# Performance work log

Measured on AMD Instinct MI355X. Metric: run time of the kernel, lower is better.

Reference implementation:

```python
import jax, jax.numpy as jnp
import numpy as np
from jax import lax

_DN = ('NCHW', 'OIHW', 'NCHW')


def _depthwise_kernel(C):
    base = jnp.array([[0.1, 0.1, 0.1], [0.1, 0.2, 0.1], [0.1, 0.1, 0.1]], jnp.float32)
    return jnp.broadcast_to(base[None, None], (C, 1, 3, 3))


def setup_inputs() -> dict:
    key = jax.random.key(0)
    k0, k1, k2 = jax.random.split(key, 3)
    T, B, C, H, W = 16, 16, 8, 128, 128
    hidden = max(1, C // 16)  # reduction_ratio = 16
    events = jax.random.normal(k0, (T, B, C, H, W), jnp.float32)
    conv_w = _depthwise_kernel(C)  # fixed neighbor kernel from _initialize_weights
    att_w1 = jax.random.normal(k1, (hidden, 2 * C), jnp.float32) / np.sqrt(2 * C)
    att_w2 = jax.random.normal(k2, (C, hidden), jnp.float32) / np.sqrt(hidden)
    return {
        'events': events,
        'conv_w': conv_w,
        'att_w1': att_w1,
        'att_w2': att_w2,
        'density_w': jnp.array(1.0, jnp.float32),
        'temporal_w': jnp.array(0.8, jnp.float32),
        'motion_w': jnp.array(0.5, jnp.float32),
    }


def _forward(events, conv_w, att_w1, att_w2, density_w, temporal_w, motion_w):
    T, B, C, H, W = events.shape
    x = events.reshape(T * B, C, H, W)
    # depthwise 3x3 neighbor conv (groups=C), batched over all T steps at once
    wi = lax.conv_general_dilated(x, conv_w, (1, 1), 'SAME',
                                  dimension_numbers=_DN, feature_group_count=C)
    # --- BALIFBetaAdaptor: max/avg pool -> 1x1 convs (== matmuls) -> sigmoid ---
    mx = jnp.max(x, axis=(2, 3))            # (TB, C)
    av = jnp.mean(x, axis=(2, 3))           # (TB, C)
    pooled = jnp.concatenate([mx, av], axis=1)  # (TB, 2C)
    h = jax.nn.relu(pooled @ att_w1.T)
    beta = (0.5 + 0.45 * jax.nn.sigmoid(h @ att_w2.T)).reshape(T, B, C, 1, 1)
    # --- LightweightEventAdaptor: density / temporal change / unfold variance ---
    density = jnp.mean(x, axis=(1, 2, 3)).reshape(T, B)
    diff = jnp.mean(jnp.abs(events[1:] - events[:-1]), axis=(2, 3, 4))
    temporal = jnp.concatenate([jnp.zeros((1, B), events.dtype), diff], axis=0)  # t=0 -> 0
    # F.unfold(k=3,pad=1) variance over dim=1 (C*9 values, unbiased) via sum-convs
    ones_k = jnp.ones((1, C, 3, 3), events.dtype)
    s1 = lax.conv_general_dilated(x, ones_k, (1, 1), 'SAME', dimension_numbers=_DN)
    s2 = lax.conv_general_dilated(x * x, ones_k, (1, 1), 'SAME', dimension_numbers=_DN)
    n = C * 9
    var = (s2 - s1 * s1 / n) / (n - 1)      # (TB,1,H,W), matches torch.var (ddof=1)
    motion = jnp.mean(var, axis=(1, 2, 3)).reshape(T, B)
    adj = jax.nn.sigmoid(density_w * density + temporal_w * temporal + motion_w * motion) * 2.0
    thr = (1.0 + adj).reshape(T, B, 1, 1, 1)  # base_threshold = 1.0
    wi = wi.reshape(T, B, C, H, W)

    # --- sequential LIF charge/fire/reset (torch.no_grad -> stop_gradient) ---
    def step(v, inp):
        w, b, th, cur = inp
        v = lax.stop_gradient(b * v + (1.0 - b) * w)              # charge
        spike = lax.stop_gradient(jnp.arctan(2.0 * (v - th)) * 0.5 + 0.5)  # atan surrogate
        v = lax.stop_gradient((1.0 - spike) * v)                  # reset (v_reset = 0)
        return v, cur * spike

    v0 = jnp.zeros((B, C, H, W), events.dtype)
    _, out = lax.scan(step, v0, (wi, beta, thr, events))
    return out  # (T,B,C,H,W)


def reference(events, conv_w, att_w1, att_w2, density_w, temporal_w, motion_w):
    return _forward(events, conv_w, att_w1, att_w2, density_w, temporal_w, motion_w)
```

## Files before the change

kernel.cpp:

```cpp
#include <hip/hip_runtime.h>
#include <math.h>

#define T_ 16
#define B_ 16
#define C_ 8
#define H_ 128
#define W_ 128
#define HW_ (H_*W_)
#define CHW_ (C_*HW_)
#define TC 4
#define NSL 16

__device__ __forceinline__ float wave_sum(float v){
    #pragma unroll
    for (int o=32;o>0;o>>=1) v += __shfl_down(v,o,64);
    return v;
}
__device__ __forceinline__ float wave_max(float v){
    #pragma unroll
    for (int o=32;o>0;o>>=1) v = fmaxf(v,__shfl_down(v,o,64));
    return v;
}

__global__ __launch_bounds__(512, 4) void stats_kernel(
    const float* __restrict__ events, float* __restrict__ partials,
    float* __restrict__ yfield)
{
    int bid   = blockIdx.x;
    int chunk = bid & 3;
    int s     = (bid >> 2) & 15;
    int b     = bid >> 6;
    int t0    = chunk * TC;
    int gh0   = s * 8;
    int tid   = threadIdx.x;
    int c     = tid >> 6;
    int lane  = tid & 63;

    __shared__ float xs[C_][1024];

    int lrow  = lane >> 3;
    int lcol0 = (lane & 7) * 16;
    int gh    = gh0 + lrow;
    float cnth = (gh==0 || gh==H_-1) ? 2.f : 3.f;
    float w0  = (lcol0==0)        ? 2.f : 3.f;
    float w15 = (lcol0+15==W_-1)  ? 2.f : 3.f;

    const float* base0 = events + (size_t)(t0*B_+b)*CHW_ + c*HW_ + gh*W_ + lcol0;
    const size_t tstep = (size_t)B_ * CHW_;

    float px[16];
    if (t0 > 0){
        const float* pp = base0 - tstep;
        #pragma unroll
        for (int e=0;e<16;e+=4){
            float4 v = *reinterpret_cast<const float4*>(pp + e);
            px[e]=v.x; px[e+1]=v.y; px[e+2]=v.z; px[e+3]=v.w;
        }
    } else {
        #pragma unroll
        for (int e=0;e<16;e++) px[e]=0.f;
    }

    #pragma unroll 1
    for (int tt=0; tt<TC; ++tt){
        int t = t0 + tt;
        const float* src = base0 + (size_t)tt*tstep;

        float cx[16];
        #pragma unroll
        for (int e=0;e<16;e+=4){
            float4 v = *reinterpret_cast<const float4*>(src + e);
            cx[e]=v.x; cx[e+1]=v.y; cx[e+2]=v.z; cx[e+3]=v.w;
        }

        float ssum=0.f, smax=-INFINITY, q=0.f, dsu=0.f;
        #pragma unroll
        for (int e=0;e<16;e++){
            float x = cx[e];
            ssum += x;
            smax = fmaxf(smax, x);
            float w = (e==0) ? w0 : ((e==15) ? w15 : 3.f);
            q = fmaf(w*x, x, q);
            dsu += fabsf(x - px[e]);
            px[e] = x;
        }

        #pragma unroll
        for (int e=0;e<16;e+=4){
            float4 v; v.x=cx[e]; v.y=cx[e+1]; v.z=cx[e+2]; v.w=cx[e+3];
            *reinterpret_cast<float4*>(&xs[c][lane*16 + e]) = v;
        }
        __syncthreads();

        {
            int p0 = tid * 2;
            float y0=0.f, y1=0.f;
            #pragma unroll
            for (int cc=0; cc<C_; cc++){
                y0 += xs[cc][p0];
                y1 += xs[cc][p0+1];
            }
            float2 yy; yy.x=y0; yy.y=y1;
            *reinterpret_cast<float2*>(yfield + (size_t)(t*B_+b)*HW_ + gh0*W_ + p0) = yy;
        }

        float rs = wave_sum(ssum);
        float rm = wave_max(smax);
        float rd = wave_sum(dsu);
        float rq = wave_sum(cnth * q);
        if (lane == 0){
            float4 o; o.x=rs; o.y=rm; o.z=rd; o.w=rq;
            *reinterpret_cast<float4*>(
                partials + (((size_t)(t*B_+b)*NSL + s)*C_ + c)*4) = o;
        }
        __syncthreads();
    }
}

__global__ __launch_bounds__(256) void m1_kernel(
    const float* __restrict__ yfield, float* __restrict__ m1p)
{
    int bid = blockIdx.x;
    int s   = bid & 7;
    int tb  = bid >> 3;
    int h0  = s*16;
    int tid = threadIdx.x;
    __shared__ float yb[18][W_];

    const float* yf = yfield + (size_t)tb*HW_;
    for (int i = tid; i < 18*32; i += 256){
        int rr = i >> 5, cc = (i & 31) * 4;
        int gh = h0 - 1 + rr;
        float4 v; v.x=0.f; v.y=0.f; v.z=0.f; v.w=0.f;
        if (gh >= 0 && gh < H_) v = *reinterpret_cast<const float4*>(yf + gh*W_ + cc);
        *reinterpret_cast<float4*>(&yb[rr][cc]) = v;
    }
    __syncthreads();

    float m1 = 0.f;
    {
        int w  = tid & 127;
        int rg = tid >> 7;
        bool hasL = (w>0), hasR = (w<W_-1);
        int base = rg*8;
        const float* row;
        row = yb[base];   float a0 = row[w] + (hasL?row[w-1]:0.f) + (hasR?row[w+1]:0.f);
        row = yb[base+1]; float a1 = row[w] + (hasL?row[w-1]:0.f) + (hasR?row[w+1]:0.f);
        #pragma unroll
        for (int i=0;i<8;i++){
            row = yb[base+2+i];
            float a2 = row[w] + (hasL?row[w-1]:0.f) + (hasR?row[w+1]:0.f);
            float s1 = a0 + a1 + a2;
            m1 = fmaf(s1, s1, m1);
            a0 = a1; a1 = a2;
        }
    }
    m1 = wave_sum(m1);
    __shared__ float red2[4];
    int lane = tid & 63, wv = tid >> 6;
    if (lane==0) red2[wv] = m1;
    __syncthreads();
    if (tid==0) m1p[bid] = (red2[0]+red2[1])+(red2[2]+red2[3]);
}

__global__ __launch_bounds__(64) void combine_kernel(
    const float* __restrict__ partials,
    const float* __restrict__ m1p,
    const float* __restrict__ att_w1,
    const float* __restrict__ att_w2,
    const float* __restrict__ dwp, const float* __restrict__ twp,
    const float* __restrict__ mwp,
    float* __restrict__ beta_out, float* __restrict__ thr_out,
    float* __restrict__ zeropad)
{
    int tb = blockIdx.x;
    int t  = tb / B_;
    int i  = threadIdx.x;
    if (tb == 0 && i < 16) zeropad[i] = 0.f;
    __shared__ float v[19];
    const float* p = partials + (size_t)tb*NSL*C_*4;
    if (i < 8){
        float acc = 0.f;
        #pragma unroll
        for (int s=0;s<NSL;s++) acc += p[(s*C_ + i)*4 + 0];
        v[i] = acc;
    } else if (i < 16){
        int c = i - 8;
        float acc = -INFINITY;
        #pragma unroll
        for (int s=0;s<NSL;s++) acc = fmaxf(acc, p[(s*C_ + c)*4 + 1]);
        v[i] = acc;
    } else if (i == 16){
        float acc = 0.f;
        for (int k=0;k<NSL*C_;k++) acc += p[k*4 + 2];
        v[16] = acc;
    } else if (i == 17){
        const float* mp = m1p + (size_t)tb*8;
        float acc = 0.f;
        #pragma unroll
        for (int k=0;k<8;k++) acc += mp[k];
        v[17] = acc;
    } else if (i == 18){
        float acc = 0.f;
        for (int k=0;k<NSL*C_;k++) acc += p[k*4 + 3];
        v[18] = acc;
    }
    __syncthreads();
    if (i == 0){
        float h1 = 0.f;
        for (int c=0;c<C_;c++) h1 += v[8+c] * att_w1[c];
        for (int c=0;c<C_;c++) h1 += (v[c]/(float)HW_) * att_w1[C_+c];
        h1 = fmaxf(h1, 0.f);
        float total = 0.f;
        for (int c=0;c<C_;c++) total += v[c];
        float density  = total / (float)CHW_;
        float temporal = (t==0) ? 0.f : v[16] / (float)CHW_;
        float motion   = (v[18] - v[17]/72.f) / 71.f / (float)HW_;
        float z = dwp[0]*density + twp[0]*temporal + mwp[0]*motion;
        float adj = 2.f / (1.f + expf(-z));
        thr_out[tb] = 1.f + adj;
        for (int c=0;c<C_;c++){
            float sg = 1.f / (1.f + expf(-(h1 * att_w2[c])));
            beta_out[tb*C_ + c] = 0.5f + 0.45f*sg;
        }
    }
}

__device__ __forceinline__ void gload16(const float* src, float* lds_dst){
    __builtin_amdgcn_global_load_lds(
        (const __attribute__((address_space(1))) unsigned int*)src,
        (__attribute__((address_space(3))) unsigned int*)lds_dst, 16, 0, 0);
}

__device__ __forceinline__ float fast_atan(float x){
    float ax = fabsf(x);
    bool inv = ax > 1.f;
    float z  = inv ? __builtin_amdgcn_rcpf(ax) : ax;
    float z2 = z*z;
    float p = -0.0117212f;
    p = fmaf(p, z2,  0.05265332f);
    p = fmaf(p, z2, -0.11643287f);
    p = fmaf(p, z2,  0.19354346f);
    p = fmaf(p, z2, -0.33262347f);
    p = fmaf(p, z2,  0.99997726f);
    p = p * z;
    float r = inv ? (1.57079632679f - p) : p;
    return copysignf(r, x);
}

#define SROWS 10

__global__ __launch_bounds__(256, 8) void lif_kernel(
    const float* __restrict__ events,
    const float* __restrict__ conv_w,
    const float* __restrict__ beta,
    const float* __restrict__ thr,
    const float* __restrict__ zeropad,
    float* __restrict__ out)
{
    int bid  = blockIdx.x;
    int hblk = bid & 15;
    int bc   = bid >> 4;
    int b = bc >> 3, c = bc & 7;
    int h0 = hblk * 8;
    int tid = threadIdx.x;
    int wv  = tid >> 6;

    float wk[9];
    #pragma unroll
    for (int k=0;k<9;k++) wk[k] = conv_w[c*9 + k];

    __shared__ float lds[2][SROWS*W_];

    int idxA = tid,        rowA = idxA >> 5, colA = (idxA & 31) * 4;
    int idxB = 256 + tid,  rowB = idxB >> 5, colB = (idxB & 31) * 4;
    int ghA = h0 - 1 + rowA;
    int ghB = h0 - 1 + rowB;
    bool okA = (ghA >= 0) && (ghA < H_);
    bool okB = (ghB >= 0) && (ghB < H_);
    const float* baseFrame = events + ((size_t)(b * C_) + c) * HW_;
    const float* srcA0 = okA ? (baseFrame + ghA*W_ + colA) : zeropad;
    const float* srcB0 = okB ? (baseFrame + ghB*W_ + colB) : zeropad;
    const size_t tstep = (size_t)B_ * CHW_;
    size_t stepA = okA ? tstep : 0;
    size_t stepB = okB ? tstep : 0;

    int w  = tid & 127;
    int rg = tid >> 7;
    int rbase = rg * 4;
    int wl = (w > 0)    ? w-1 : 0;
    int wr = (w < W_-1) ? w+1 : W_-1;
    bool hasL = (w > 0), hasR = (w < W_-1);

    float v[4];
    #pragma unroll
    for (int i=0;i<4;i++) v[i] = 0.f;

    gload16(srcA0, &lds[0][wv*256]);
    if (wv == 0) gload16(srcB0, &lds[0][1024]);

    const float* bp = beta + (b*C_ + c);
    const float* tp = thr + b;
    float bv = bp[0];
    float th = tp[0];

    for (int t = 0; t < T_; ++t){
        int cur = t & 1, nxt = cur ^ 1;
        __syncthreads();

        if (t + 1 < T_){
            gload16(srcA0 + (size_t)(t+1)*stepA, &lds[nxt][wv*256]);
            if (wv == 0) gload16(srcB0 + (size_t)(t+1)*stepB, &lds[nxt][1024]);
        }
        float bvn = (t+1 < T_) ? bp[(size_t)(t+1)*B_*C_] : 0.f;
        float thn = (t+1 < T_) ? tp[(size_t)(t+1)*B_]    : 0.f;

        const float* L = &lds[cur][0];
        float omb = 1.f - bv;
        float* op = out + ((size_t)(t*B_+b)*C_ + c)*HW_ + h0*W_;

        const float* row0 = L + rbase*W_;
        const float* row1 = row0 + W_;
        float la = hasL ? row0[wl] : 0.f;  float ma = row0[w];  float ra = hasR ? row0[wr] : 0.f;
        float lb = hasL ? row1[wl] : 0.f;  float mb = row1[w];  float rb = hasR ? row1[wr] : 0.f;

        #pragma unroll
        for (int i=0;i<4;i++){
            const float* rowc = L + (rbase+2+i)*W_;
            float lc = hasL ? rowc[wl] : 0.f;
            float mc = rowc[w];
            float rc = hasR ? rowc[wr] : 0.f;
            float wi = wk[0]*la + wk[1]*ma + wk[2]*ra
                     + wk[3]*lb + wk[4]*mb + wk[5]*rb
                     + wk[6]*lc + wk[7]*mc + wk[8]*rc;
            float vv = fmaf(bv, v[i], omb*wi);
            float sp = fast_atan(2.f*(vv - th))*0.5f + 0.5f;
            __builtin_nontemporal_store(mb * sp, &op[(rbase+i)*W_ + w]);
            v[i] = (1.f - sp) * vv;
            la=lb; ma=mb; ra=rb; lb=lc; mb=mc; rb=rc;
        }
        __syncthreads();

        bv = bvn; th = thn;
    }
}

extern "C" void kernel_launch(void* const* d_in, const int* in_sizes, int n_in,
                              void* d_out, int out_size, void* d_ws, size_t ws_size,
                              hipStream_t stream)
{
    const float* events = (const float*)d_in[0];
    const float* conv_w = (const float*)d_in[1];
    const float* att_w1 = (const float*)d_in[2];
    const float* att_w2 = (const float*)d_in[3];
    const float* dwp    = (const float*)d_in[4];
    const float* twp    = (const float*)d_in[5];
    const float* mwp    = (const float*)d_in[6];
    float* out = (float*)d_out;

    float* ws       = (float*)d_ws;
    float* partials = ws;
    float* m1p      = partials + (size_t)T_*B_*NSL*C_*4;
    float* beta     = m1p + (size_t)T_*B_*8;
    float* thr      = beta + (size_t)T_*B_*C_;
    float* zeropad  = thr + T_*B_;
    float* yfield   = zeropad + 16;

    stats_kernel  <<<B_*NSL*4,  512, 0, stream>>>(events, partials, yfield);
    m1_kernel     <<<T_*B_*8,   256, 0, stream>>>(yfield, m1p);
    combine_kernel<<<T_*B_,     64,  0, stream>>>(partials, m1p, att_w1, att_w2,
                                                  dwp, twp, mwp, beta, thr, zeropad);
    lif_kernel    <<<B_*C_*16,  256, 0, stream>>>(events, conv_w, beta, thr, zeropad, out);
}
```

Measured before the change: 95.37 us.

## Restructure LIF kernel: register-prefetch triple-buffered LDS, float4 tiles, cheaper atan

```diff
diff --git a/kernel.cpp b/kernel.cpp
--- a/kernel.cpp
+++ b/kernel.cpp
@@ -10,6 +10,8 @@
 #define CHW_ (C_*HW_)
 #define TC 4
 #define NSL 16
+
+typedef float __attribute__((ext_vector_type(4))) f32x4;
 
 __device__ __forceinline__ float wave_sum(float v){
     #pragma unroll
@@ -170,13 +172,11 @@
     const float* __restrict__ att_w2,
     const float* __restrict__ dwp, const float* __restrict__ twp,
     const float* __restrict__ mwp,
-    float* __restrict__ beta_out, float* __restrict__ thr_out,
-    float* __restrict__ zeropad)
+    float* __restrict__ beta_out, float* __restrict__ thr_out)
 {
     int tb = blockIdx.x;
     int t  = tb / B_;
     int i  = threadIdx.x;
-    if (tb == 0 && i < 16) zeropad[i] = 0.f;
     __shared__ float v[19];
     const float* p = partials + (size_t)tb*NSL*C_*4;
     if (i < 8){
@@ -226,36 +226,27 @@
     }
 }
 
-__device__ __forceinline__ void gload16(const float* src, float* lds_dst){
-    __builtin_amdgcn_global_load_lds(
-        (const __attribute__((address_space(1))) unsigned int*)src,
-        (__attribute__((address_space(3))) unsigned int*)lds_dst, 16, 0, 0);
-}
-
-__device__ __forceinline__ float fast_atan(float x){
+__device__ __forceinline__ float fast_atan5(float x){
     float ax = fabsf(x);
     bool inv = ax > 1.f;
     float z  = inv ? __builtin_amdgcn_rcpf(ax) : ax;
     float z2 = z*z;
-    float p = -0.0117212f;
-    p = fmaf(p, z2,  0.05265332f);
-    p = fmaf(p, z2, -0.11643287f);
-    p = fmaf(p, z2,  0.19354346f);
-    p = fmaf(p, z2, -0.33262347f);
-    p = fmaf(p, z2,  0.99997726f);
+    float p = 0.0793331f;
+    p = fmaf(p, z2, -0.2886790f);
+    p = fmaf(p, z2,  0.9953540f);
     p = p * z;
     float r = inv ? (1.57079632679f - p) : p;
     return copysignf(r, x);
 }
 
-#define SROWS 10
-
-__global__ __launch_bounds__(256, 8) void lif_kernel(
+#define LST 136
+#define SR_ 10
+
+__global__ __launch_bounds__(256, 4) void lif_kernel(
     const float* __restrict__ events,
     const float* __restrict__ conv_w,
     const float* __restrict__ beta,
     const float* __restrict__ thr,
-    const float* __restrict__ zeropad,
     float* __restrict__ out)
 {
     int bid  = blockIdx.x;
@@ -264,84 +255,124 @@
     int b = bc >> 3, c = bc & 7;
     int h0 = hblk * 8;
     int tid = threadIdx.x;
-    int wv  = tid >> 6;
 
     float wk[9];
     #pragma unroll
     for (int k=0;k<9;k++) wk[k] = conv_w[c*9 + k];
 
-    __shared__ float lds[2][SROWS*W_];
-
-    int idxA = tid,        rowA = idxA >> 5, colA = (idxA & 31) * 4;
-    int idxB = 256 + tid,  rowB = idxB >> 5, colB = (idxB & 31) * 4;
+    __shared__ float lds[3][SR_*LST];
+
+    if (tid < 60){
+        int bsel = tid / 20, j = tid % 20;
+        int row = j >> 1, col = (j & 1) ? 132 : 3;
+        lds[bsel][row*LST + col] = 0.f;
+    }
+
+    int rowA = tid >> 5,        cgA = tid & 31;
+    int rowB = (256+tid) >> 5,  cgB = tid & 31;
     int ghA = h0 - 1 + rowA;
     int ghB = h0 - 1 + rowB;
     bool okA = (ghA >= 0) && (ghA < H_);
-    bool okB = (ghB >= 0) && (ghB < H_);
-    const float* baseFrame = events + ((size_t)(b * C_) + c) * HW_;
-    const float* srcA0 = okA ? (baseFrame + ghA*W_ + colA) : zeropad;
-    const float* srcB0 = okB ? (baseFrame + ghB*W_ + colB) : zeropad;
+    bool okB = (tid < 64) && (ghB >= 0) && (ghB < H_);
+    const float* baseFrame = events + ((size_t)(b*C_) + c) * HW_;
+    const float* srcA = baseFrame + ghA*W_ + cgA*4;
+    const float* srcB = baseFrame + ghB*W_ + cgB*4;
     const size_t tstep = (size_t)B_ * CHW_;
-    size_t stepA = okA ? tstep : 0;
-    size_t stepB = okB ? tstep : 0;
-
-    int w  = tid & 127;
-    int rg = tid >> 7;
-    int rbase = rg * 4;
-    int wl = (w > 0)    ? w-1 : 0;
-    int wr = (w < W_-1) ? w+1 : W_-1;
-    bool hasL = (w > 0), hasR = (w < W_-1);
+    int ldsA = rowA*LST + 4 + cgA*4;
+    int ldsB = rowB*LST + 4 + cgB*4;
+
+    int cg = tid & 31;
+    int r  = tid >> 5;
+    int cbase = 4 + cg*4;
 
     float v[4];
     #pragma unroll
     for (int i=0;i<4;i++) v[i] = 0.f;
 
-    gload16(srcA0, &lds[0][wv*256]);
-    if (wv == 0) gload16(srcB0, &lds[0][1024]);
+    float4 z4; z4.x=0.f; z4.y=0.f; z4.z=0.f; z4.w=0.f;
+
+    {
+        float4 sa = okA ? *reinterpret_cast<const float4*>(srcA) : z4;
+        float4 sb = okB ? *reinterpret_cast<const float4*>(srcB) : z4;
+        *reinterpret_cast<float4*>(&lds[0][ldsA]) = sa;
+        if (tid < 64) *reinterpret_cast<float4*>(&lds[0][ldsB]) = sb;
+    }
+    float4 rA = okA ? *reinterpret_cast<const float4*>(srcA + tstep) : z4;
+    float4 rB = okB ? *reinterpret_cast<const float4*>(srcB + tstep) : z4;
+    __syncthreads();
 
     const float* bp = beta + (b*C_ + c);
     const float* tp = thr + b;
     float bv = bp[0];
     float th = tp[0];
 
+    int cur = 0;
+    #pragma unroll 1
     for (int t = 0; t < T_; ++t){
-        int cur = t & 1, nxt = cur ^ 1;
-        __syncthreads();
+        int nxt = cur + 1; if (nxt == 3) nxt = 0;
 
         if (t + 1 < T_){
-            gload16(srcA0 + (size_t)(t+1)*stepA, &lds[nxt][wv*256]);
-            if (wv == 0) gload16(srcB0 + (size_t)(t+1)*stepB, &lds[nxt][1024]);
+            *reinterpret_cast<float4*>(&lds[nxt][ldsA]) = rA;
+            if (tid < 64) *reinterpret_cast<float4*>(&lds[nxt][ldsB]) = rB;
+        }
+        if (t + 2 < T_){
+            rA = okA ? *reinterpret_cast<const float4*>(srcA + (size_t)(t+2)*tstep) : z4;
+            rB = okB ? *reinterpret_cast<const float4*>(srcB + (size_t)(t+2)*tstep) : z4;
         }
         float bvn = (t+1 < T_) ? bp[(size_t)(t+1)*B_*C_] : 0.f;
         float thn = (t+1 < T_) ? tp[(size_t)(t+1)*B_]    : 0.f;
 
-        const float* L = &lds[cur][0];
+        const float* Lr = &lds[cur][r*LST + cbase];
+        float4 um = *reinterpret_cast<const float4*>(Lr);
+        float  lm = Lr[-1],        rm = Lr[4];
+        const float* Lc = Lr + LST;
+        float4 uc = *reinterpret_cast<const float4*>(Lc);
+        float  lc = Lc[-1],        rc = Lc[4];
+        const float* Lp = Lc + LST;
+        float4 up = *reinterpret_cast<const float4*>(Lp);
+        float  lp = Lp[-1],        rp = Lp[4];
+
         float omb = 1.f - bv;
-        float* op = out + ((size_t)(t*B_+b)*C_ + c)*HW_ + h0*W_;
-
-        const float* row0 = L + rbase*W_;
-        const float* row1 = row0 + W_;
-        float la = hasL ? row0[wl] : 0.f;  float ma = row0[w];  float ra = hasR ? row0[wr] : 0.f;
-        float lb = hasL ? row1[wl] : 0.f;  float mb = row1[w];  float rb = hasR ? row1[wr] : 0.f;
-
-        #pragma unroll
-        for (int i=0;i<4;i++){
-            const float* rowc = L + (rbase+2+i)*W_;
-            float lc = hasL ? rowc[wl] : 0.f;
-            float mc = rowc[w];
-            float rc = hasR ? rowc[wr] : 0.f;
-            float wi = wk[0]*la + wk[1]*ma + wk[2]*ra
-                     + wk[3]*lb + wk[4]*mb + wk[5]*rb
-                     + wk[6]*lc + wk[7]*mc + wk[8]*rc;
-            float vv = fmaf(bv, v[i], omb*wi);
-            float sp = fast_atan(2.f*(vv - th))*0.5f + 0.5f;
-            __builtin_nontemporal_store(mb * sp, &op[(rbase+i)*W_ + w]);
-            v[i] = (1.f - sp) * vv;
-            la=lb; ma=mb; ra=rb; lb=lc; mb=mc; rb=rc;
-        }
+        float th2 = 2.f * th;
+
+        float wi0 = wk[0]*lm   + wk[1]*um.x + wk[2]*um.y
+                  + wk[3]*lc   + wk[4]*uc.x + wk[5]*uc.y
+                  + wk[6]*lp   + wk[7]*up.x + wk[8]*up.y;
+        float wi1 = wk[0]*um.x + wk[1]*um.y + wk[2]*um.z
+                  + wk[3]*uc.x + wk[4]*uc.y + wk[5]*uc.z
+                  + wk[6]*up.x + wk[7]*up.y + wk[8]*up.z;
+        float wi2 = wk[0]*um.y + wk[1]*um.z + wk[2]*um.w
+                  + wk[3]*uc.y + wk[4]*uc.z + wk[5]*uc.w
+                  + wk[6]*up.y + wk[7]*up.z + wk[8]*up.w;
+        float wi3 = wk[0]*um.z + wk[1]*um.w + wk[2]*rm
+                  + wk[3]*uc.z + wk[4]*uc.w + wk[5]*rc
+                  + wk[6]*up.z + wk[7]*up.w + wk[8]*rp;
+
+        float vv0 = fmaf(bv, v[0], omb*wi0);
+        float vv1 = fmaf(bv, v[1], omb*wi1);
+        float vv2 = fmaf(bv, v[2], omb*wi2);
+        float vv3 = fmaf(bv, v[3], omb*wi3);
+
+        float sp0 = fmaf(fast_atan5(fmaf(2.f, vv0, -th2)), 0.5f, 0.5f);
+        float sp1 = fmaf(fast_atan5(fmaf(2.f, vv1, -th2)), 0.5f, 0.5f);
+        float sp2 = fmaf(fast_atan5(fmaf(2.f, vv2, -th2)), 0.5f, 0.5f);
+        float sp3 = fmaf(fast_atan5(fmaf(2.f, vv3, -th2)), 0.5f, 0.5f);
+
+        f32x4 o;
+        o.x = uc.x * sp0;  o.y = uc.y * sp1;
+        o.z = uc.z * sp2;  o.w = uc.w * sp3;
+        f32x4* op = reinterpret_cast<f32x4*>(
+            out + ((size_t)(t*B_+b)*C_ + c)*HW_ + (h0+r)*W_ + cg*4);
+        __builtin_nontemporal_store(o, op);
+
+        v[0] = (1.f - sp0) * vv0;
+        v[1] = (1.f - sp1) * vv1;
+        v[2] = (1.f - sp2) * vv2;
+        v[3] = (1.f - sp3) * vv3;
+
         __syncthreads();
-
         bv = bvn; th = thn;
+        cur = nxt;
     }
 }
 
@@ -363,12 +394,11 @@
     float* m1p      = partials + (size_t)T_*B_*NSL*C_*4;
     float* beta     = m1p + (size_t)T_*B_*8;
     float* thr      = beta + (size_t)T_*B_*C_;
-    float* zeropad  = thr + T_*B_;
-    float* yfield   = zeropad + 16;
+    float* yfield   = thr + T_*B_;
 
     stats_kernel  <<<B_*NSL*4,  512, 0, stream>>>(events, partials, yfield);
     m1_kernel     <<<T_*B_*8,   256, 0, stream>>>(yfield, m1p);
     combine_kernel<<<T_*B_,     64,  0, stream>>>(partials, m1p, att_w1, att_w2,
-                                                  dwp, twp, mwp, beta, thr, zeropad);
-    lif_kernel    <<<B_*C_*16,  256, 0, stream>>>(events, conv_w, beta, thr, zeropad, out);
-}
+                                                  dwp, twp, mwp, beta, thr);
+    lif_kernel    <<<B_*C_*16,  256, 0, stream>>>(events, conv_w, beta, thr, out);
+}
```

New measurement: 98.32 us. +3.1%, slower.
